# Optimization experiments

Measured on AMD Instinct MI355X. Metric: run time of the kernel, lower is better.

The kernel has to match this reference:

```python
import jax, jax.numpy as jnp
import numpy as np

TOPK = 20
BN_EPS = 1e-5
NEG_SLOPE = 0.2  # DGL GAT default leaky_relu slope


def setup_inputs() -> dict:
    B, N, Ft, D = 128, 512, 64, 64
    key = jax.random.key(0)
    ks = jax.random.split(key, 6)
    return {
        "data": jax.random.normal(ks[0], (B, N, Ft), jnp.float32),
        "emb": jax.random.normal(ks[1], (N, D), jnp.float32) * 0.5,
        "fc_w": jax.random.normal(ks[2], (D, Ft), jnp.float32) * (1.0 / np.sqrt(Ft)),
        "fc_b": jnp.zeros((D,), jnp.float32),
        "attn_w": jax.random.normal(ks[3], (4 * D,), jnp.float32) * (1.0 / np.sqrt(4 * D)),
        "attn_b": jnp.zeros((), jnp.float32),
        "bn_gamma": jnp.ones((D,), jnp.float32),
        "bn_beta": jnp.zeros((D,), jnp.float32),
        "out_w": jax.random.normal(ks[4], (D,), jnp.float32) * (1.0 / np.sqrt(D)),
        "out_b": jnp.zeros((), jnp.float32),
    }


def reference(data, emb, fc_w, fc_b, attn_w, attn_b, bn_gamma, bn_beta, out_w, out_b):
    B, N, Ft = data.shape
    D = emb.shape[-1]

    # --- dynamic graph build from detached embeddings (cosine-sim topk) ---
    w = jax.lax.stop_gradient(emb)
    nrm = jnp.linalg.norm(w, axis=-1)
    cos = (w @ w.T) / (nrm[:, None] * nrm[None, :])      # [N, N]
    _, topk_idx = jax.lax.top_k(cos, TOPK)               # [N, TOPK]
    src = topk_idx.reshape(-1)                           # gated_j (message sources)
    dst = jnp.tile(jnp.arange(N), TOPK)                  # gated_i = arange(N).repeat(1,topk).flatten()

    # --- GAT layer: z = W x + b ; edge score from concat([z, emb]) at both ends ---
    z = jnp.einsum("bnf,df->bnd", data, fc_w) + fc_b     # [B, N, D]
    key_feat = jnp.concatenate([z, jnp.broadcast_to(emb, (B, N, D))], axis=-1)  # [B, N, 2D]
    a_src, a_dst = attn_w[: 2 * D], attn_w[2 * D :]
    s_src = jnp.einsum("bnd,d->bn", key_feat, a_src)
    s_dst = jnp.einsum("bnd,d->bn", key_feat, a_dst)
    e = jax.nn.leaky_relu(s_src[:, src] + s_dst[:, dst] + attn_b, NEG_SLOPE)    # [B, E]

    # segment softmax over incoming edges of each dst node (same edges every batch)
    m = jnp.full((B, N), -jnp.inf, e.dtype).at[:, dst].max(e)
    p = jnp.exp(e - m[:, dst])
    denom = jnp.zeros((B, N), e.dtype).at[:, dst].add(p)
    alpha = p / denom[:, dst]                            # [B, E]

    # scatter-aggregate messages
    h = jnp.zeros_like(z).at[:, dst].add(alpha[..., None] * z[:, src])          # [B, N, D]

    # --- trailing dense: mul by embedding, BatchNorm1d over channel D, relu, linear ---
    rst = h * emb[None]                                  # [B, N, D]
    mu = rst.mean(axis=(0, 1))
    var = rst.var(axis=(0, 1))
    rst = jax.nn.relu((rst - mu) / jnp.sqrt(var + BN_EPS) * bn_gamma + bn_beta)
    out = jnp.einsum("bnd,d->bn", rst, out_w) + out_b    # [B, N]
    return out
```

## Files before the change

kernel.cpp:

```cpp
#include <hip/hip_runtime.h>
#include <hip/hip_bf16.h>

#define NN 512
#define DD 64
#define TOPK 20
#define BB 128

__global__ __launch_bounds__(256) void kpre(const float* __restrict__ emb,
                                            const float* __restrict__ attn_w,
                                            double* __restrict__ nrm,
                                            float* __restrict__ es_src,
                                            float* __restrict__ es_dst,
                                            double* __restrict__ gstats) {
    const int bid = blockIdx.x, t = threadIdx.x;
    if (bid < 2) {
        const int j = bid * 256 + t;
        const float4* e4 = (const float4*)emb;
        double s = 0.0;
        #pragma unroll
        for (int c = 0; c < 16; ++c) {
            const float4 v = e4[j * 16 + c];
            const double vx = v.x, vy = v.y, vz = v.z, vw = v.w;
            s += vx * vx; s += vy * vy; s += vz * vz; s += vw * vw;
        }
        nrm[j] = sqrt(s);
        if (bid == 0 && t < 128) gstats[t] = 0.0;
    } else {
        const int j = (bid - 2) * 256 + t;
        float s1 = 0.f, s2 = 0.f;
        #pragma unroll
        for (int c = 0; c < 64; ++c) {
            const float w = emb[j * 64 + c];
            s1 += w * attn_w[64 + c];
            s2 += w * attn_w[192 + c];
        }
        es_src[j] = s1;
        es_dst[j] = s2;
    }
}

__global__ __launch_bounds__(256) void L1_fused(const float* __restrict__ data,
                                                const float* __restrict__ emb,
                                                const float* __restrict__ fc_w,
                                                const float* __restrict__ fc_b,
                                                const float* __restrict__ attn_w,
                                                const double* __restrict__ nrmArr,
                                                float* __restrict__ z,
                                                float* __restrict__ zsrc,
                                                float* __restrict__ zdst,
                                                int* __restrict__ topk) {
    __shared__ __align__(16) char smem[36864];
    const int bid = blockIdx.x, t = threadIdx.x;
    const int wid = t >> 6, lane = t & 63;

    if (bid < 128) {
        float4* lds4 = (float4*)smem;
        float4* wis4 = (float4*)(smem + 34816);
        const int i = bid * 4 + wid;
        const float4* e4 = (const float4*)emb;

        if (t < 64) wis4[t] = e4[(bid * 4 + (t >> 4)) * 16 + (t & 15)];
        __syncthreads();

        const double nrm_i = nrmArr[i];

        double v[8];
        for (int tile = 0; tile < 4; ++tile) {
            __syncthreads();
            for (int m = t; m < 2048; m += 256) {
                const int row = m >> 4, c = m & 15;
                lds4[row * 17 + c] = e4[tile * 2048 + m];
            }
            __syncthreads();
            #pragma unroll
            for (int rb = 0; rb < 2; ++rb) {
                const int slot = tile * 2 + rb;
                const int rl = rb * 64 + lane;
                double dot = 0.0;
                #pragma unroll
                for (int c = 0; c < 16; ++c) {
                    const float4 vv = lds4[rl * 17 + c];
                    const float4 w  = wis4[wid * 16 + c];
                    dot += (double)w.x * (double)vv.x;
                    dot += (double)w.y * (double)vv.y;
                    dot += (double)w.z * (double)vv.z;
                    dot += (double)w.w * (double)vv.w;
                }
                v[slot] = dot / (nrm_i * nrmArr[slot * 64 + lane]);
            }
        }

        for (int k = 0; k < TOPK; ++k) {
            double bv = v[0]; int bs = 0;
            #pragma unroll
            for (int s = 1; s < 8; ++s) if (v[s] > bv) { bv = v[s]; bs = s; }
            int bi = bs * 64 + lane;
            #pragma unroll
            for (int off = 32; off > 0; off >>= 1) {
                double ov = __shfl_xor(bv, off);
                int    oi = __shfl_xor(bi, off);
                if (ov > bv || (ov == bv && oi < bi)) { bv = ov; bi = oi; }
            }
            if (lane == 0) topk[i * TOPK + k] = bi;
            if ((bi & 63) == lane) v[bi >> 6] = -1e300;
        }
    } else {
        float* WsT = (float*)smem;
        const float4* fcw4 = (const float4*)fc_w;
        for (int m = t; m < 1024; m += 256) {
            const int d = m >> 4, f4 = m & 15;
            float4 v = fcw4[d * 16 + f4];
            WsT[(f4 * 4 + 0) * 65 + d] = v.x;
            WsT[(f4 * 4 + 1) * 65 + d] = v.y;
            WsT[(f4 * 4 + 2) * 65 + d] = v.z;
            WsT[(f4 * 4 + 3) * 65 + d] = v.w;
        }
        __syncthreads();

        float Breg[64];
        #pragma unroll
        for (int f = 0; f < 64; ++f) Breg[f] = WsT[f * 65 + lane];

        const float bias = fc_b[lane];
        const float aw0  = attn_w[lane];
        const float aw2  = attn_w[128 + lane];
        const long rbase = ((long)(bid - 128) * 4 + wid) * 32;

        #pragma unroll
        for (int g = 0; g < 4; ++g) {
            float a8[8];
            #pragma unroll
            for (int r = 0; r < 8; ++r)
                a8[r] = data[(rbase + g * 8 + r) * 64 + lane];
            #pragma unroll
            for (int r = 0; r < 8; ++r) {
                float acc = 0.f;
                #pragma unroll
                for (int f = 0; f < 64; ++f) {
                    const float af = __int_as_float(
                        __builtin_amdgcn_readlane(__float_as_int(a8[r]), f));
                    acc = fmaf(af, Breg[f], acc);
                }
                const float zb = acc + bias;
                const long row = rbase + g * 8 + r;
                z[row * 64 + lane] = zb;
                float p1 = zb * aw0, p2 = zb * aw2;
                #pragma unroll
                for (int off = 32; off > 0; off >>= 1) {
                    p1 += __shfl_xor(p1, off);
                    p2 += __shfl_xor(p2, off);
                }
                if (lane == 0) { zsrc[row] = p1; zdst[row] = p2; }
            }
        }
    }
}

__global__ __launch_bounds__(256) void k3_attn(const float* __restrict__ z,
                                               const float* __restrict__ zsrc,
                                               const float* __restrict__ zdst,
                                               const float* __restrict__ es_src,
                                               const float* __restrict__ es_dst,
                                               const int* __restrict__ topk,
                                               const float* __restrict__ emb,
                                               const float* __restrict__ attn_b_p,
                                               float* __restrict__ rst,
                                               double* __restrict__ gstats) {
    __shared__ float  zs[512 * 16];
    __shared__ double alf_pool[2560];
    __shared__ unsigned short sIdx[256 * 20];
    float* alf = (float*)alf_pool;

    const int b    = blockIdx.x >> 2;
    const int dq   = blockIdx.x & 3;
    const int doff = dq * 16;
    const int t    = threadIdx.x;
    const float attn_b = *attn_b_p;
    const long b512 = (long)b * NN;

    float4* zs4 = (float4*)zs;
    for (int m = t; m < 2048; m += 256) {
        const int n = m >> 2, c4i = m & 3;
        zs4[m] = *(const float4*)(z + (b512 + n) * 64 + doff + c4i * 4);
    }
    __syncthreads();

    const int c4 = t & 3;
    const int rq = t >> 2;
    double s1[4] = {0,0,0,0}, s2[4] = {0,0,0,0};

    for (int chunk = 0; chunk < 2; ++chunk) {
        {
            const int n = chunk * 256 + t;
            const float sd = zdst[b512 + n] + es_dst[n] + attn_b;
            float ev[TOPK];
            float m0 = -1e30f;
            #pragma unroll
            for (int tt = 0; tt < TOPK; ++tt) {
                const int s = topk[n + tt * NN];
                sIdx[t * TOPK + tt] = (unsigned short)s;
                float e = zsrc[b512 + s] + es_src[s] + sd;
                e = (e >= 0.f) ? e : 0.2f * e;
                ev[tt] = e;
                m0 = fmaxf(m0, e);
            }
            float dsum = 0.f;
            #pragma unroll
            for (int tt = 0; tt < TOPK; ++tt) { ev[tt] = __expf(ev[tt] - m0); dsum += ev[tt]; }
            const float inv = 1.0f / dsum;
            #pragma unroll
            for (int tt = 0; tt < TOPK; ++tt) alf[t * TOPK + tt] = ev[tt] * inv;
        }
        __syncthreads();

        #pragma unroll
        for (int it = 0; it < 4; ++it) {
            const int nl = it * 64 + rq;
            const int n  = chunk * 256 + nl;
            float4 acc = {0.f, 0.f, 0.f, 0.f};
            #pragma unroll
            for (int tt = 0; tt < TOPK; ++tt) {
                const float a = alf[nl * TOPK + tt];
                const float4 zv = zs4[(int)sIdx[nl * TOPK + tt] * 4 + c4];
                acc.x += a * zv.x; acc.y += a * zv.y; acc.z += a * zv.z; acc.w += a * zv.w;
            }
            const float4 ev = *(const float4*)&emb[n * 64 + doff + c4 * 4];
            float4 r;
            r.x = acc.x * ev.x; r.y = acc.y * ev.y; r.z = acc.z * ev.z; r.w = acc.w * ev.w;
            *(float4*)&rst[(b512 + n) * 64 + doff + c4 * 4] = r;
            s1[0] += (double)r.x; s2[0] += (double)r.x * (double)r.x;
            s1[1] += (double)r.y; s2[1] += (double)r.y * (double)r.y;
            s1[2] += (double)r.z; s2[2] += (double)r.z * (double)r.z;
            s1[3] += (double)r.w; s2[3] += (double)r.w * (double)r.w;
        }
        __syncthreads();
    }

    double* r1 = alf_pool;
    double* r2 = alf_pool + 1024;
    #pragma unroll
    for (int j = 0; j < 4; ++j) {
        r1[(c4 * 4 + j) * 64 + rq] = s1[j];
        r2[(c4 * 4 + j) * 64 + rq] = s2[j];
    }
    __syncthreads();
    if (t < 16) {
        double a = 0.0, bb = 0.0;
        for (int q = 0; q < 64; ++q) { a += r1[t * 64 + q]; bb += r2[t * 64 + q]; }
        atomicAdd(&gstats[doff + t], a);
        atomicAdd(&gstats[64 + doff + t], bb);
    }
}

__global__ __launch_bounds__(256) void k5_out(const float* __restrict__ rst,
                                              const double* __restrict__ gstats,
                                              const float* __restrict__ gamma,
                                              const float* __restrict__ beta,
                                              const float* __restrict__ out_w,
                                              const float* __restrict__ out_b_p,
                                              float* __restrict__ out) {
    __shared__ float scv[64], biv[64];
    const int t = threadIdx.x;
    if (t < 64) {
        const double M = (double)BB * (double)NN;
        const double s  = gstats[t];
        const double s2 = gstats[64 + t];
        const double mu  = s / M;
        const double var = s2 / M - mu * mu;
        const float scale = (float)((double)gamma[t] / sqrt(var + 1e-5));
        scv[t] = scale;
        biv[t] = beta[t] - (float)mu * scale;
    }
    __syncthreads();

    const int wid = t >> 6, lane = t & 63;
    const float sc = scv[lane], bi = biv[lane], ow = out_w[lane];
    const float ob = *out_b_p;
    const long rowbase = (long)blockIdx.x * 16 + wid * 4;
    float v[4];
    #pragma unroll
    for (int rr = 0; rr < 4; ++rr)
        v[rr] = fmaxf(rst[(rowbase + rr) * 64 + lane] * sc + bi, 0.f) * ow;
    #pragma unroll
    for (int off = 32; off > 0; off >>= 1)
        #pragma unroll
        for (int rr = 0; rr < 4; ++rr) v[rr] += __shfl_down(v[rr], off);
    if (lane == 0)
        #pragma unroll
        for (int rr = 0; rr < 4; ++rr) out[rowbase + rr] = v[rr] + ob;
}

extern "C" void kernel_launch(void* const* d_in, const int* in_sizes, int n_in,
                              void* d_out, int out_size, void* d_ws, size_t ws_size,
                              hipStream_t stream) {
    const float* data   = (const float*)d_in[0];
    const float* emb    = (const float*)d_in[1];
    const float* fc_w   = (const float*)d_in[2];
    const float* fc_b   = (const float*)d_in[3];
    const float* attn_w = (const float*)d_in[4];
    const float* attn_b = (const float*)d_in[5];
    const float* gamma  = (const float*)d_in[6];
    const float* beta   = (const float*)d_in[7];
    const float* out_w  = (const float*)d_in[8];
    const float* out_b  = (const float*)d_in[9];
    float* out = (float*)d_out;

    char* ws = (char*)d_ws;
    float*  z      = (float*) (ws + 0);
    float*  rst    = (float*) (ws + 16777216);
    float*  zsrc   = (float*) (ws + 33554432);
    float*  zdst   = (float*) (ws + 33816576);
    int*    topk   = (int*)   (ws + 34078720);
    float*  es_src = (float*) (ws + 34119680);
    float*  es_dst = (float*) (ws + 34121728);
    double* gstats = (double*)(ws + 34123776);
    double* nrm    = (double*)(ws + 34124800);

    kpre<<<4, 256, 0, stream>>>(emb, attn_w, nrm, es_src, es_dst, gstats);
    L1_fused<<<640, 256, 0, stream>>>(data, emb, fc_w, fc_b, attn_w, nrm,
                                      z, zsrc, zdst, topk);
    k3_attn<<<BB * 4, 256, 0, stream>>>(z, zsrc, zdst, es_src, es_dst, topk, emb,
                                        attn_b, rst, gstats);
    k5_out<<<4096, 256, 0, stream>>>(rst, gstats, gamma, beta, out_w, out_b, out);
}
```

Before: 159.4 us.

## Split cosine-sim into tiled Gram blocks fused with linear pass, separate top-k kernel

The Gram matrix of embeddings is now computed in 32x32 tiles by 256 extra blocks of the fused kernel, alongside the linear projection. The norm and attention-score preprocessing moves into that same launch, which removes the kpre kernel. Top-k selection moves to a new ksel kernel that reads the stored double-precision Gram matrix and normalises by the norms. The goal is to spread the fp64 dot-product work across more blocks and drop one launch dependency, at the cost of a 2 MB intermediate round-trip and an extra kernel launch.

```diff
diff --git a/kernel.cpp b/kernel.cpp
--- a/kernel.cpp
+++ b/kernel.cpp
@@ -5,106 +5,25 @@
 #define DD 64
 #define TOPK 20
 #define BB 128
-
-__global__ __launch_bounds__(256) void kpre(const float* __restrict__ emb,
-                                            const float* __restrict__ attn_w,
-                                            double* __restrict__ nrm,
-                                            float* __restrict__ es_src,
-                                            float* __restrict__ es_dst,
-                                            double* __restrict__ gstats) {
-    const int bid = blockIdx.x, t = threadIdx.x;
-    if (bid < 2) {
-        const int j = bid * 256 + t;
-        const float4* e4 = (const float4*)emb;
-        double s = 0.0;
-        #pragma unroll
-        for (int c = 0; c < 16; ++c) {
-            const float4 v = e4[j * 16 + c];
-            const double vx = v.x, vy = v.y, vz = v.z, vw = v.w;
-            s += vx * vx; s += vy * vy; s += vz * vz; s += vw * vw;
-        }
-        nrm[j] = sqrt(s);
-        if (bid == 0 && t < 128) gstats[t] = 0.0;
-    } else {
-        const int j = (bid - 2) * 256 + t;
-        float s1 = 0.f, s2 = 0.f;
-        #pragma unroll
-        for (int c = 0; c < 64; ++c) {
-            const float w = emb[j * 64 + c];
-            s1 += w * attn_w[64 + c];
-            s2 += w * attn_w[192 + c];
-        }
-        es_src[j] = s1;
-        es_dst[j] = s2;
-    }
-}
 
 __global__ __launch_bounds__(256) void L1_fused(const float* __restrict__ data,
                                                 const float* __restrict__ emb,
                                                 const float* __restrict__ fc_w,
                                                 const float* __restrict__ fc_b,
                                                 const float* __restrict__ attn_w,
-                                                const double* __restrict__ nrmArr,
                                                 float* __restrict__ z,
                                                 float* __restrict__ zsrc,
                                                 float* __restrict__ zdst,
-                                                int* __restrict__ topk) {
-    __shared__ __align__(16) char smem[36864];
+                                                double* __restrict__ cosM,
+                                                double* __restrict__ nrm,
+                                                float* __restrict__ es_src,
+                                                float* __restrict__ es_dst,
+                                                double* __restrict__ gstats) {
+    __shared__ __align__(16) char smem[17408];
     const int bid = blockIdx.x, t = threadIdx.x;
     const int wid = t >> 6, lane = t & 63;
 
-    if (bid < 128) {
-        float4* lds4 = (float4*)smem;
-        float4* wis4 = (float4*)(smem + 34816);
-        const int i = bid * 4 + wid;
-        const float4* e4 = (const float4*)emb;
-
-        if (t < 64) wis4[t] = e4[(bid * 4 + (t >> 4)) * 16 + (t & 15)];
-        __syncthreads();
-
-        const double nrm_i = nrmArr[i];
-
-        double v[8];
-        for (int tile = 0; tile < 4; ++tile) {
-            __syncthreads();
-            for (int m = t; m < 2048; m += 256) {
-                const int row = m >> 4, c = m & 15;
-                lds4[row * 17 + c] = e4[tile * 2048 + m];
-            }
-            __syncthreads();
-            #pragma unroll
-            for (int rb = 0; rb < 2; ++rb) {
-                const int slot = tile * 2 + rb;
-                const int rl = rb * 64 + lane;
-                double dot = 0.0;
-                #pragma unroll
-                for (int c = 0; c < 16; ++c) {
-                    const float4 vv = lds4[rl * 17 + c];
-                    const float4 w  = wis4[wid * 16 + c];
-                    dot += (double)w.x * (double)vv.x;
-                    dot += (double)w.y * (double)vv.y;
-                    dot += (double)w.z * (double)vv.z;
-                    dot += (double)w.w * (double)vv.w;
-                }
-                v[slot] = dot / (nrm_i * nrmArr[slot * 64 + lane]);
-            }
-        }
-
-        for (int k = 0; k < TOPK; ++k) {
-            double bv = v[0]; int bs = 0;
-            #pragma unroll
-            for (int s = 1; s < 8; ++s) if (v[s] > bv) { bv = v[s]; bs = s; }
-            int bi = bs * 64 + lane;
-            #pragma unroll
-            for (int off = 32; off > 0; off >>= 1) {
-                double ov = __shfl_xor(bv, off);
-                int    oi = __shfl_xor(bi, off);
-                if (ov > bv || (ov == bv && oi < bi)) { bv = ov; bi = oi; }
-            }
-            if (lane == 0) topk[i * TOPK + k] = bi;
-            if ((bi & 63) == lane) v[bi >> 6] = -1e300;
-        }
-    } else {
+    if (bid < 512) {
         float* WsT = (float*)smem;
         const float4* fcw4 = (const float4*)fc_w;
         for (int m = t; m < 1024; m += 256) {
@@ -124,7 +43,7 @@
         const float bias = fc_b[lane];
         const float aw0  = attn_w[lane];
         const float aw2  = attn_w[128 + lane];
-        const long rbase = ((long)(bid - 128) * 4 + wid) * 32;
+        const long rbase = ((long)bid * 4 + wid) * 32;
 
         #pragma unroll
         for (int g = 0; g < 4; ++g) {
@@ -153,6 +72,93 @@
                 if (lane == 0) { zsrc[row] = p1; zdst[row] = p2; }
             }
         }
+    } else if (bid < 768) {
+        const int tile = bid - 512;
+        const int bi0 = (tile >> 4) * 32;
+        const int bj0 = (tile & 15) * 32;
+        float4* A4 = (float4*)smem;
+        float4* B4 = (float4*)(smem + 8704);
+        const float4* e4 = (const float4*)emb;
+
+        for (int m = t; m < 512; m += 256) {
+            const int r = m >> 4, c = m & 15;
+            A4[r * 17 + c] = e4[(bi0 + r) * 16 + c];
+            B4[r * 17 + c] = e4[(bj0 + r) * 16 + c];
+        }
+        __syncthreads();
+
+        const int tr = t >> 4, tc = t & 15;
+        #pragma unroll
+        for (int rr = 0; rr < 2; ++rr) {
+            #pragma unroll
+            for (int cc = 0; cc < 2; ++cc) {
+                const int r  = tr + rr * 16;
+                const int cl = tc + cc * 16;
+                double dot = 0.0;
+                #pragma unroll
+                for (int c = 0; c < 16; ++c) {
+                    const float4 a = A4[r * 17 + c];
+                    const float4 b = B4[cl * 17 + c];
+                    dot += (double)a.x * (double)b.x;
+                    dot += (double)a.y * (double)b.y;
+                    dot += (double)a.z * (double)b.z;
+                    dot += (double)a.w * (double)b.w;
+                }
+                cosM[(long)(bi0 + r) * NN + (bj0 + cl)] = dot;
+            }
+        }
+    } else if (bid < 770) {
+        const int j = (bid - 768) * 256 + t;
+        const float4* e4 = (const float4*)emb;
+        double s = 0.0;
+        #pragma unroll
+        for (int c = 0; c < 16; ++c) {
+            const float4 v = e4[j * 16 + c];
+            const double vx = v.x, vy = v.y, vz = v.z, vw = v.w;
+            s += vx * vx; s += vy * vy; s += vz * vz; s += vw * vw;
+        }
+        nrm[j] = sqrt(s);
+        if (bid == 768 && t < 128) gstats[t] = 0.0;
+    } else {
+        const int j = (bid - 770) * 256 + t;
+        float s1 = 0.f, s2 = 0.f;
+        #pragma unroll
+        for (int c = 0; c < 64; ++c) {
+            const float w = emb[j * 64 + c];
+            s1 += w * attn_w[64 + c];
+            s2 += w * attn_w[192 + c];
+        }
+        es_src[j] = s1;
+        es_dst[j] = s2;
+    }
+}
+
+__global__ __launch_bounds__(256) void ksel(const double* __restrict__ cosM,
+                                            const double* __restrict__ nrmArr,
+                                            int* __restrict__ topk) {
+    const int t = threadIdx.x;
+    const int wid = t >> 6, lane = t & 63;
+    const int i = blockIdx.x * 4 + wid;
+
+    const double nrm_i = nrmArr[i];
+    double v[8];
+    #pragma unroll
+    for (int s = 0; s < 8; ++s)
+        v[s] = cosM[(long)i * NN + s * 64 + lane] / (nrm_i * nrmArr[s * 64 + lane]);
+
+    for (int k = 0; k < TOPK; ++k) {
+        double bv = v[0]; int bs = 0;
+        #pragma unroll
+        for (int s = 1; s < 8; ++s) if (v[s] > bv) { bv = v[s]; bs = s; }
+        int bi = bs * 64 + lane;
+        #pragma unroll
+        for (int off = 32; off > 0; off >>= 1) {
+            double ov = __shfl_xor(bv, off);
+            int    oi = __shfl_xor(bi, off);
+            if (ov > bv || (ov == bv && oi < bi)) { bv = ov; bi = oi; }
+        }
+        if (lane == 0) topk[i * TOPK + k] = bi;
+        if ((bi & 63) == lane) v[bi >> 6] = -1e300;
     }
 }
 
@@ -315,10 +321,12 @@
     float*  es_dst = (float*) (ws + 34121728);
     double* gstats = (double*)(ws + 34123776);
     double* nrm    = (double*)(ws + 34124800);
-
-    kpre<<<4, 256, 0, stream>>>(emb, attn_w, nrm, es_src, es_dst, gstats);
-    L1_fused<<<640, 256, 0, stream>>>(data, emb, fc_w, fc_b, attn_w, nrm,
-                                      z, zsrc, zdst, topk);
+    double* cosM   = (double*)(ws + 34131968);
+
+    L1_fused<<<772, 256, 0, stream>>>(data, emb, fc_w, fc_b, attn_w,
+                                      z, zsrc, zdst, cosM, nrm,
+                                      es_src, es_dst, gstats);
+    ksel<<<128, 256, 0, stream>>>(cosM, nrm, topk);
     k3_attn<<<BB * 4, 256, 0, stream>>>(z, zsrc, zdst, es_src, es_dst, topk, emb,
                                         attn_b, rst, gstats);
     k5_out<<<4096, 256, 0, stream>>>(rst, gstats, gamma, beta, out_w, out_b, out);
```

New measurement: 178.6 us. 12.1% more time.
